# Optimization experiments

Hardware: AMD Instinct MI355X
Metric: run time of the kernel (lower is better)

The kernel has to match this reference:

```python
import jax, jax.numpy as jnp
import numpy as np

PENALTY = -100.0  # reset penalty used by the torch module


def log_g(x):
    # torch: where(x >= 0, log(relu(x) + 0.5), -softplus(-x))
    return jnp.where(x >= 0, jnp.log(jax.nn.relu(x) + 0.5), -jax.nn.softplus(-x))


def setup_inputs() -> dict:
    key = jax.random.key(0)
    k1, k2, k3 = jax.random.split(key, 3)
    B, S, D = 4, 8192, 1024
    x = jax.random.normal(k1, (B, S, D), dtype=jnp.float32)
    W = jax.random.normal(k2, (D, 2 * D), dtype=jnp.float32) * (1.0 / np.sqrt(D))
    input_ids = jax.random.randint(k3, (B, S), 0, 32000, dtype=jnp.int64)
    return {"x": x, "W": W, "input_ids": input_ids}


def reference(x, W, input_ids):
    # x: [B,S,D], W: [D,2D] (to_hidden_and_gate, no bias), proj_out=False -> Identity
    hg = jnp.einsum("bsd,de->bse", x, W)            # [B,S,2D]
    hidden, gate = jnp.split(hg, 2, axis=-1)          # each [B,S,D]

    pad_mask = input_ids == 0                         # [B,S]

    log_coeffs = -jax.nn.softplus(gate)               # log(1 - z)
    log_z = -jax.nn.softplus(-gate)                   # log z
    log_values = log_z + log_g(hidden)                # log(z * h_tilde)

    # reset at positions following a pad token (shifted mask)
    reset = jnp.pad(pad_mask[:, :-1], ((0, 0), (1, 0)))[:, :, None]  # [B,S,1]

    lc = jnp.where(reset, PENALTY, log_coeffs)
    a_star = jnp.cumsum(lc, axis=1)
    lv = jnp.where(reset, PENALTY, log_values)
    log_h = a_star + jax.lax.cumlogsumexp(lv - a_star, axis=1)
    out = jnp.exp(log_h)                              # [B,S,D]

    next_prev_hidden = jnp.where(pad_mask[:, -1:, None], 0.0, out[:, -1:])
    return out, next_prev_hidden
```

## Files before the change

### kernel.cpp

```cpp
#include <hip/hip_runtime.h>
#include <hip/hip_fp16.h>
#include <math.h>

#define S_LEN 8192
#define D_DIM 1024
#define B_DIM 4
#define M_DIM (B_DIM * S_LEN)
#define BSD   ((size_t)M_DIM * D_DIM)
#define CHN   (B_DIM * D_DIM)
#define CHUNK 64
#define NCH   (S_LEN / CHUNK)

typedef _Float16 f16x8 __attribute__((ext_vector_type(8)));
typedef __attribute__((ext_vector_type(4))) float f32x4;
typedef unsigned int u32;

__device__ __forceinline__ u32 pk2h(float a, float b) {
    auto h = __builtin_amdgcn_cvt_pkrtz(a, b);
    u32 r; __builtin_memcpy(&r, &h, 4); return r;
}

__device__ __forceinline__ void gload16(const void* g, void* l) {
    __builtin_amdgcn_global_load_lds(
        (const __attribute__((address_space(1))) u32*)g,
        (__attribute__((address_space(3))) u32*)l,
        16, 0, 0);
}

__global__ __launch_bounds__(256) void w_to_f16t(
    const float* __restrict__ W, unsigned short* __restrict__ Wt)
{
    __shared__ float T[64][65];
    const int t  = threadIdx.x;
    const int n0 = (int)blockIdx.x * 64;
    const int k0 = (int)blockIdx.y * 64;
    #pragma unroll
    for (int p = 0; p < 4; ++p) {
        int u = p * 256 + t;
        int r = u >> 4, c4 = (u & 15) * 4;
        float4 v = *(const float4*)&W[(size_t)(k0 + r) * 2048 + n0 + c4];
        T[r][c4 + 0] = v.x; T[r][c4 + 1] = v.y;
        T[r][c4 + 2] = v.z; T[r][c4 + 3] = v.w;
    }
    __syncthreads();
    #pragma unroll
    for (int p = 0; p < 2; ++p) {
        int u = p * 256 + t;
        int n = u >> 3, kc = (u & 7) * 8;
        u32 out[4];
        #pragma unroll
        for (int j = 0; j < 4; ++j)
            out[j] = pk2h(T[kc + 2 * j][n], T[kc + 2 * j + 1][n]);
        *(uint4*)&Wt[(size_t)(n0 + n) * 1024 + k0 + kc] = *(uint4*)out;
    }
}

__global__ __launch_bounds__(256) void x_to_f16sw(
    const float* __restrict__ x, unsigned short* __restrict__ xh)
{
    int tid = (int)blockIdx.x * 256 + threadIdx.x;
    int m  = tid >> 7;
    int cg = tid & 127;
    const float4* src = (const float4*)&x[(size_t)m * 1024 + cg * 8];
    float4 v0 = src[0], v1 = src[1];
    u32 o[4] = { pk2h(v0.x, v0.y), pk2h(v0.z, v0.w),
                 pk2h(v1.x, v1.y), pk2h(v1.z, v1.w) };
    int j   = cg & 7;
    int cgd = (cg & ~7) | (j ^ (m & 7));
    *(uint4*)&xh[(size_t)m * 1024 + cgd * 8] = *(uint4*)o;
}

__global__ __launch_bounds__(512, 2) void gemm_8p(
    const unsigned short* __restrict__ xh, const unsigned short* __restrict__ Wt,
    const int* __restrict__ ids, u32* __restrict__ P)
{
    __shared__ __align__(16) unsigned short Ah[2 * 256 * 64];

    const int t    = threadIdx.x;
    const int lane = t & 63;
    const int wid  = t >> 6;
    const int wm   = wid >> 2;
    const int wd   = wid & 3;

    const int lin  = (int)blockIdx.x;
    const int xcd  = lin & 7;
    const int slot = lin >> 3;
    const int m0   = (xcd * 16 + (slot >> 3)) * 256;
    const int c0   = (slot & 7) * 128;

    f32x4 accH[8][2], accG[8][2];
    #pragma unroll
    for (int i = 0; i < 8; ++i)
        #pragma unroll
        for (int j = 0; j < 2; ++j) {
            accH[i][j] = (f32x4)0.0f;
            accG[i][j] = (f32x4)0.0f;
        }

    auto stageA = [&](int kb, int buf, int half) {
        char* Ad = (char*)Ah + (buf << 15) + (half << 14);
        #pragma unroll
        for (int i = 0; i < 2; ++i) {
            int sl  = i * 512 + t;
            int row = half * 128 + (sl >> 3);
            int c   = sl & 7;
            const unsigned short* src =
                xh + ((size_t)(m0 + row) << 10) + kb + (c << 3);
            gload16(src, Ad + (size_t)sl * 16);
        }
    };

    auto readA = [&](const char* Ab, int kk, f16x8 a[8]) {
        int chunk = kk * 4 + (lane >> 4);
        #pragma unroll
        for (int mf = 0; mf < 8; ++mf) {
            int row = wm * 128 + mf * 16 + (lane & 15);
            a[mf] = *(const f16x8*)(Ab + row * 128 + ((chunk ^ (row & 7)) << 4));
        }
    };

    auto loadB = [&](f16x8 b[2], int kb, int kk, int hg) {
        int chunk = kk * 4 + (lane >> 4);
        #pragma unroll
        for (int df = 0; df < 2; ++df) {
            int col = wd * 32 + df * 16 + (lane & 15);
            b[df] = *(const f16x8*)(Wt + ((size_t)(hg * 1024 + c0 + col) << 10)
                                       + kb + (chunk << 3));
        }
    };

    #define MMA_CLUSTER(ACC, AV, BV)                                       \
        __builtin_amdgcn_s_setprio(1);                                     \
        _Pragma("unroll")                                                  \
        for (int mf = 0; mf < 8; ++mf)                                     \
            _Pragma("unroll")                                              \
            for (int df = 0; df < 2; ++df)                                 \
                ACC[mf][df] = __builtin_amdgcn_mfma_f32_16x16x32_f16(      \
                    AV[mf], BV[df], ACC[mf][df], 0, 0, 0);                 \
        __builtin_amdgcn_s_setprio(0);

    f16x8 a0[8], a1[8], bh0[2], bg0[2], bh1[2], bg1[2];

    loadB(bh0, 0, 0, 0); loadB(bg0, 0, 0, 1); loadB(bh1, 0, 1, 0);
    stageA(0, 0, 0); stageA(0, 0, 1);
    asm volatile("s_waitcnt vmcnt(0)" ::: "memory");
    __builtin_amdgcn_sched_barrier(0);
    __builtin_amdgcn_s_barrier();

    for (int tt = 0; tt < 16; ++tt) {
        const int buf   = tt & 1;
        const int kbc   = tt << 6;
        const int kbn   = (tt + 1) << 6;
        const bool more = tt < 15;
        const char* Ab = (const char*)Ah + (buf << 15);

        if (tt) { MMA_CLUSTER(accG, a1, bg1) }
        loadB(bg1, kbc, 1, 1);
        if (more) { stageA(kbn, buf ^ 1, 0); stageA(kbn, buf ^ 1, 1); }
        readA(Ab, 0, a0);
        asm volatile("s_waitcnt lgkmcnt(0)" ::: "memory");
        __builtin_amdgcn_sched_barrier(0);
        MMA_CLUSTER(accH, a0, bh0)
        if (more) loadB(bh0, kbn, 0, 0);
        readA(Ab, 1, a1);
        MMA_CLUSTER(accG, a0, bg0)
        if (more) loadB(bg0, kbn, 0, 1);
        asm volatile("s_waitcnt lgkmcnt(0)" ::: "memory");
        __builtin_amdgcn_sched_barrier(0);
        MMA_CLUSTER(accH, a1, bh1)
        if (more) loadB(bh1, kbn, 1, 0);
        if (more) {
            asm volatile("s_waitcnt vmcnt(6)" ::: "memory");
            __builtin_amdgcn_sched_barrier(0);
            __builtin_amdgcn_s_barrier();
        }
    }
    MMA_CLUSTER(accG, a1, bg1)
    #undef MMA_CLUSTER

    #pragma unroll
    for (int mf = 0; mf < 8; ++mf) {
        int mbase = m0 + wm * 128 + mf * 16 + (lane >> 4) * 4;
        #pragma unroll
        for (int r = 0; r < 4; ++r) {
            int m = mbase + r;
            int b = m >> 13;
            int s = m & 8191;
            bool reset = (s > 0) && (ids[b * S_LEN + s - 1] == 0);
            #pragma unroll
            for (int df = 0; df < 2; ++df) {
                int d = c0 + wd * 32 + df * 16 + (lane & 15);
                float hid = accH[mf][df][r];
                float g   = accG[mf][df][r];
                float eg  = __expf(-g);
                float z   = 1.0f / (1.0f + eg);
                float c   = eg * z;
                float gt  = (hid >= 0.0f) ? (hid + 0.5f)
                                          : 1.0f / (1.0f + __expf(-hid));
                float v   = z * gt;
                if (reset) { c = 0.0f; v = 0.0f; }
                __half2 h2 = __floats2half2_rn(c, v);
                u32 packed;
                __builtin_memcpy(&packed, &h2, 4);
                P[(size_t)m * D_DIM + d] = packed;
            }
        }
    }
}

__global__ __launch_bounds__(256, 3) void gemm_fb(
    const float* __restrict__ x, const unsigned short* __restrict__ Wt,
    const int* __restrict__ ids, u32* __restrict__ P)
{
    __shared__ __align__(16) unsigned short Ah[128 * 64];
    __shared__ __align__(16) unsigned short Bt[2 * 64 * 64];

    const int t    = threadIdx.x;
    const int lane = t & 63;
    const int wid  = t >> 6;
    const int wm   = wid >> 1;
    const int wd   = wid & 1;

    const int lin  = (int)blockIdx.y * (int)gridDim.x + (int)blockIdx.x;
    const int xcd  = lin & 7;
    const int slot = lin >> 3;
    const int m0   = (xcd * 32 + (slot >> 4)) * 128;
    const int c0   = (slot & 15) * 64;

    f32x4 accH[4][2], accG[4][2];
    #pragma unroll
    for (int i = 0; i < 4; ++i)
        #pragma unroll
        for (int j = 0; j < 2; ++j) {
            accH[i][j] = (f32x4)0.0f;
            accG[i][j] = (f32x4)0.0f;
        }

    for (int kb = 0; kb < 1024; kb += 64) {
        __syncthreads();
        #pragma unroll
        for (int i = 0; i < 4; ++i) {
            int slotb = wid * 256 + i * 64;
            int sl  = slotb + lane;
            int hg  = sl >> 9;
            int col = (sl >> 3) & 63;
            int kc  = (sl & 7) ^ (col & 7);
            const unsigned short* src =
                Wt + ((size_t)(hg * 1024 + c0 + col) << 10) + kb + (kc << 3);
            gload16(src, (char*)Bt + (size_t)slotb * 16);
        }
        #pragma unroll
        for (int p = 0; p < 8; ++p) {
            int s   = p * 256 + t;
            int row = s >> 4;
            int c4  = s & 15;
            float4 v = *(const float4*)&x[(size_t)(m0 + row) * 1024 + kb + c4 * 4];
            uint2 h;
            h.x = pk2h(v.x, v.y);
            h.y = pk2h(v.z, v.w);
            int byte = row * 128 + ((((c4 >> 1) ^ (row & 7))) << 4) + ((c4 & 1) << 3);
            *(uint2*)((char*)Ah + byte) = h;
        }
        __syncthreads();
        #pragma unroll
        for (int kk = 0; kk < 2; ++kk) {
            f16x8 bh[2], bg[2];
            #pragma unroll
            for (int df = 0; df < 2; ++df) {
                int col = wd * 32 + df * 16 + (lane & 15);
                int chunk = kk * 4 + (lane >> 4);
                int byte = col * 128 + ((chunk ^ (col & 7)) << 4);
                bh[df] = *(const f16x8*)((const char*)Bt + byte);
                bg[df] = *(const f16x8*)((const char*)Bt + 8192 + byte);
            }
            #pragma unroll
            for (int mf = 0; mf < 4; ++mf) {
                int row = wm * 64 + mf * 16 + (lane & 15);
                int chunk = kk * 4 + (lane >> 4);
                int byte = row * 128 + ((chunk ^ (row & 7)) << 4);
                f16x8 a = *(const f16x8*)((const char*)Ah + byte);
                #pragma unroll
                for (int df = 0; df < 2; ++df) {
                    accH[mf][df] = __builtin_amdgcn_mfma_f32_16x16x32_f16(
                        a, bh[df], accH[mf][df], 0, 0, 0);
                    accG[mf][df] = __builtin_amdgcn_mfma_f32_16x16x32_f16(
                        a, bg[df], accG[mf][df], 0, 0, 0);
                }
            }
        }
    }

    #pragma unroll
    for (int mf = 0; mf < 4; ++mf) {
        int mbase = m0 + wm * 64 + mf * 16 + (lane >> 4) * 4;
        #pragma unroll
        for (int r = 0; r < 4; ++r) {
            int m = mbase + r;
            int b = m >> 13;
            int s = m & 8191;
            bool reset = (s > 0) && (ids[b * S_LEN + s - 1] == 0);
            #pragma unroll
            for (int df = 0; df < 2; ++df) {
                int d = c0 + wd * 32 + df * 16 + (lane & 15);
                float hid = accH[mf][df][r];
                float g   = accG[mf][df][r];
                float eg  = __expf(-g);
                float z   = 1.0f / (1.0f + eg);
                float c   = eg * z;
                float gt  = (hid >= 0.0f) ? (hid + 0.5f)
                                          : 1.0f / (1.0f + __expf(-hid));
                float v   = z * gt;
                if (reset) { c = 0.0f; v = 0.0f; }
                __half2 h2 = __floats2half2_rn(c, v);
                u32 packed;
                __builtin_memcpy(&packed, &h2, 4);
                P[(size_t)m * D_DIM + d] = packed;
            }
        }
    }
}

__global__ __launch_bounds__(256) void scan_phase_a(
    const u32* __restrict__ P,
    float* __restrict__ Cp, float* __restrict__ Lp)
{
    int ch0 = (blockIdx.x * 256 + threadIdx.x) * 4;
    int c   = blockIdx.y;
    int b   = ch0 >> 10;
    int d0  = ch0 & 1023;
    size_t base = (size_t)b * S_LEN * D_DIM + d0;
    int s0 = c * CHUNK;

    float C[4] = {1.f, 1.f, 1.f, 1.f};
    float H[4] = {0.f, 0.f, 0.f, 0.f};
    for (int s = 0; s < CHUNK; ++s) {
        uint4 q = *(const uint4*)&P[base + (size_t)(s0 + s) * D_DIM];
        u32 qs[4] = {q.x, q.y, q.z, q.w};
        #pragma unroll
        for (int j = 0; j < 4; ++j) {
            __half2 h2;
            __builtin_memcpy(&h2, &qs[j], 4);
            float cc = __low2float(h2);
            float vv = __high2float(h2);
            H[j] = fmaf(cc, H[j], vv);
            C[j] *= cc;
        }
    }
    *(float4*)&Cp[c * CHN + ch0] = *(float4*)C;
    *(float4*)&Lp[c * CHN + ch0] = *(float4*)H;
}

__global__ __launch_bounds__(256) void scan_phase_b(
    const float* __restrict__ Cp, const float* __restrict__ Lp,
    float* __restrict__ carry)
{
    int ch = blockIdx.x * 256 + threadIdx.x;
    float h = 0.0f;
    for (int c = 0; c < NCH; ++c) {
        carry[c * CHN + ch] = h;
        h = fmaf(Cp[c * CHN + ch], h, Lp[c * CHN + ch]);
    }
}

__global__ __launch_bounds__(256) void scan_phase_c(
    u32* __restrict__ Pio,
    const float* __restrict__ carry,
    const int* __restrict__ ids)
{
    int ch0 = (blockIdx.x * 256 + threadIdx.x) * 4;
    int c   = blockIdx.y;
    int b   = ch0 >> 10;
    int d0  = ch0 & 1023;
    size_t base = (size_t)b * S_LEN * D_DIM + d0;
    int s0 = c * CHUNK;

    float H[4];
    *(float4*)H = *(const float4*)&carry[c * CHN + ch0];

    for (int s = 0; s < CHUNK; ++s) {
        size_t idx = base + (size_t)(s0 + s) * D_DIM;
        uint4 q = *(const uint4*)&Pio[idx];
        u32 qs[4] = {q.x, q.y, q.z, q.w};
        u32 os[4];
        #pragma unroll
        for (int j = 0; j < 4; ++j) {
            __half2 h2;
            __builtin_memcpy(&h2, &qs[j], 4);
            float cc = __low2float(h2);
            float vv = __high2float(h2);
            H[j] = fmaf(cc, H[j], vv);
            os[j] = __float_as_uint(H[j]);
        }
        *(uint4*)&Pio[idx] = *(uint4*)os;
    }
    if (c == NCH - 1) {
        bool pad = (ids[b * S_LEN + (S_LEN - 1)] == 0);
        u32 os[4];
        #pragma unroll
        for (int j = 0; j < 4; ++j)
            os[j] = __float_as_uint(pad ? 0.0f : H[j]);
        *(uint4*)&Pio[BSD + (size_t)b * D_DIM + d0] = *(uint4*)os;
    }
}

extern "C" void kernel_launch(void* const* d_in, const int* in_sizes, int n_in,
                              void* d_out, int out_size, void* d_ws, size_t ws_size,
                              hipStream_t stream) {
    const float* x   = (const float*)d_in[0];
    const float* W   = (const float*)d_in[1];
    const int*   ids = (const int*)d_in[2];

    u32* P = (u32*)d_out;
    unsigned short* Wt = (unsigned short*)d_ws;
    float* Cp    = (float*)((char*)d_ws + (size_t) 4 * 1024 * 1024);
    float* Lp    = (float*)((char*)d_ws + (size_t) 6 * 1024 * 1024);
    float* carry = (float*)((char*)d_ws + (size_t) 8 * 1024 * 1024);
    unsigned short* xh = (unsigned short*)((char*)d_ws + (size_t)10 * 1024 * 1024);
    const size_t need = (size_t)10 * 1024 * 1024 + BSD * 2;

    w_to_f16t<<<dim3(32, 16), 256, 0, stream>>>(W, Wt);

    if (ws_size >= need) {
        x_to_f16sw<<<(M_DIM * 128) / 256, 256, 0, stream>>>(x, xh);
        gemm_8p<<<1024, 512, 0, stream>>>(xh, Wt, ids, P);
    } else {
        dim3 ggrid(D_DIM / 64, M_DIM / 128);
        gemm_fb<<<ggrid, 256, 0, stream>>>(x, Wt, ids, P);
    }

    dim3 sgrid(CHN / 1024, NCH);
    scan_phase_a<<<sgrid, 256, 0, stream>>>(P, Cp, Lp);
    scan_phase_b<<<CHN / 256, 256, 0, stream>>>(Cp, Lp, carry);
    scan_phase_c<<<sgrid, 256, 0, stream>>>(P, carry, ids);
}
```

Before: 304.5 us.

## Restructure fused GEMM to stage both A and B tiles through LDS

Replaces the 512-thread GEMM, which read B fragments directly from global memory with a 64-wide k step, with a 256-thread kernel that stages both x and W tiles into LDS with a 32-wide k step and double buffering. The block tile narrows to 64 output columns, the grid doubles, and the block-to-XCD mapping now assigns columns by XCD. The XOR swizzle on x is removed. The goal is to cut redundant global B loads and simplify the pipeline, but dropping the swizzle risks LDS bank conflicts on the 64-byte row stride, and the full vmcnt(0) wait each iteration reduces overlap between loads and MFMA.

Result: slower. 312.9 us (+2.8%).

```diff
diff --git a/kernel.cpp b/kernel.cpp
--- a/kernel.cpp
+++ b/kernel.cpp
@@ -55,7 +55,7 @@
     }
 }
 
-__global__ __launch_bounds__(256) void x_to_f16sw(
+__global__ __launch_bounds__(256) void x_to_f16(
     const float* __restrict__ x, unsigned short* __restrict__ xh)
 {
     int tid = (int)blockIdx.x * 256 + threadIdx.x;
@@ -65,28 +65,27 @@
     float4 v0 = src[0], v1 = src[1];
     u32 o[4] = { pk2h(v0.x, v0.y), pk2h(v0.z, v0.w),
                  pk2h(v1.x, v1.y), pk2h(v1.z, v1.w) };
-    int j   = cg & 7;
-    int cgd = (cg & ~7) | (j ^ (m & 7));
-    *(uint4*)&xh[(size_t)m * 1024 + cgd * 8] = *(uint4*)o;
-}
-
-__global__ __launch_bounds__(512, 2) void gemm_8p(
+    *(uint4*)&xh[(size_t)m * 1024 + cg * 8] = *(uint4*)o;
+}
+
+__global__ __launch_bounds__(256, 2) void gemm_dc(
     const unsigned short* __restrict__ xh, const unsigned short* __restrict__ Wt,
     const int* __restrict__ ids, u32* __restrict__ P)
 {
-    __shared__ __align__(16) unsigned short Ah[2 * 256 * 64];
+    __shared__ __align__(16) unsigned short Ah[2 * 256 * 32];
+    __shared__ __align__(16) unsigned short Bh[2 * 128 * 32];
 
     const int t    = threadIdx.x;
     const int lane = t & 63;
     const int wid  = t >> 6;
-    const int wm   = wid >> 2;
-    const int wd   = wid & 3;
+    const int wm   = wid >> 1;
+    const int wd   = wid & 1;
 
     const int lin  = (int)blockIdx.x;
     const int xcd  = lin & 7;
     const int slot = lin >> 3;
-    const int m0   = (xcd * 16 + (slot >> 3)) * 256;
-    const int c0   = (slot & 7) * 128;
+    const int m0   = (slot & 127) * 256;
+    const int c0   = (((slot >> 7) << 3) | xcd) * 64;
 
     f32x4 accH[8][2], accG[8][2];
     #pragma unroll
@@ -97,35 +96,44 @@
             accG[i][j] = (f32x4)0.0f;
         }
 
-    auto stageA = [&](int kb, int buf, int half) {
-        char* Ad = (char*)Ah + (buf << 15) + (half << 14);
-        #pragma unroll
-        for (int i = 0; i < 2; ++i) {
-            int sl  = i * 512 + t;
-            int row = half * 128 + (sl >> 3);
-            int c   = sl & 7;
+    auto stageA = [&](int kb, int buf) {
+        char* Ad = (char*)Ah + buf * 16384;
+        #pragma unroll
+        for (int i = 0; i < 4; ++i) {
+            int sl  = i * 256 + t;
+            int row = sl >> 2;
+            int c   = sl & 3;
             const unsigned short* src =
                 xh + ((size_t)(m0 + row) << 10) + kb + (c << 3);
-            gload16(src, Ad + (size_t)sl * 16);
+            gload16(src, Ad + sl * 16);
         }
     };
-
-    auto readA = [&](const char* Ab, int kk, f16x8 a[8]) {
-        int chunk = kk * 4 + (lane >> 4);
+    auto stageB = [&](int kb, int buf) {
+        char* Bd = (char*)Bh + buf * 8192;
+        #pragma unroll
+        for (int i = 0; i < 2; ++i) {
+            int sl  = i * 256 + t;
+            int row = sl >> 2;
+            int c   = sl & 3;
+            int grow = (row >> 6) * 1024 + c0 + (row & 63);
+            const unsigned short* src =
+                Wt + ((size_t)grow << 10) + kb + (c << 3);
+            gload16(src, Bd + sl * 16);
+        }
+    };
+
+    auto readA = [&](const char* Ab, f16x8 a[8]) {
         #pragma unroll
         for (int mf = 0; mf < 8; ++mf) {
             int row = wm * 128 + mf * 16 + (lane & 15);
-            a[mf] = *(const f16x8*)(Ab + row * 128 + ((chunk ^ (row & 7)) << 4));
+            a[mf] = *(const f16x8*)(Ab + row * 64 + ((lane >> 4) << 4));
         }
     };
-
-    auto loadB = [&](f16x8 b[2], int kb, int kk, int hg) {
-        int chunk = kk * 4 + (lane >> 4);
+    auto readB = [&](const char* Bb, int hg, f16x8 b[2]) {
         #pragma unroll
         for (int df = 0; df < 2; ++df) {
-            int col = wd * 32 + df * 16 + (lane & 15);
-            b[df] = *(const f16x8*)(Wt + ((size_t)(hg * 1024 + c0 + col) << 10)
-                                       + kb + (chunk << 3));
+            int row = hg * 64 + wd * 32 + df * 16 + (lane & 15);
+            b[df] = *(const f16x8*)(Bb + row * 64 + ((lane >> 4) << 4));
         }
     };
 
@@ -139,43 +147,32 @@
                     AV[mf], BV[df], ACC[mf][df], 0, 0, 0);                 \
         __builtin_amdgcn_s_setprio(0);
 
-    f16x8 a0[8], a1[8], bh0[2], bg0[2], bh1[2], bg1[2];
-
-    loadB(bh0, 0, 0, 0); loadB(bg0, 0, 0, 1); loadB(bh1, 0, 1, 0);
-    stageA(0, 0, 0); stageA(0, 0, 1);
+    stageA(0, 0); stageB(0, 0);
     asm volatile("s_waitcnt vmcnt(0)" ::: "memory");
     __builtin_amdgcn_sched_barrier(0);
     __builtin_amdgcn_s_barrier();
 
-    for (int tt = 0; tt < 16; ++tt) {
+    for (int tt = 0; tt < 32; ++tt) {
         const int buf   = tt & 1;
-        const int kbc   = tt << 6;
-        const int kbn   = (tt + 1) << 6;
-        const bool more = tt < 15;
-        const char* Ab = (const char*)Ah + (buf << 15);
-
-        if (tt) { MMA_CLUSTER(accG, a1, bg1) }
-        loadB(bg1, kbc, 1, 1);
-        if (more) { stageA(kbn, buf ^ 1, 0); stageA(kbn, buf ^ 1, 1); }
-        readA(Ab, 0, a0);
+        const bool more = tt < 31;
+        const char* Ab = (const char*)Ah + buf * 16384;
+        const char* Bb = (const char*)Bh + buf * 8192;
+        f16x8 a[8], bh[2], bg[2];
+
+        if (more) { stageA((tt + 1) * 32, buf ^ 1); stageB((tt + 1) * 32, buf ^ 1); }
+        readA(Ab, a); readB(Bb, 0, bh); readB(Bb, 1, bg);
+        asm volatile("s_waitcnt lgkmcnt(2)" ::: "memory");
+        __builtin_amdgcn_sched_barrier(0);
+        MMA_CLUSTER(accH, a, bh)
         asm volatile("s_waitcnt lgkmcnt(0)" ::: "memory");
         __builtin_amdgcn_sched_barrier(0);
-        MMA_CLUSTER(accH, a0, bh0)
-        if (more) loadB(bh0, kbn, 0, 0);
-        readA(Ab, 1, a1);
-        MMA_CLUSTER(accG, a0, bg0)
-        if (more) loadB(bg0, kbn, 0, 1);
-        asm volatile("s_waitcnt lgkmcnt(0)" ::: "memory");
-        __builtin_amdgcn_sched_barrier(0);
-        MMA_CLUSTER(accH, a1, bh1)
-        if (more) loadB(bh1, kbn, 1, 0);
+        MMA_CLUSTER(accG, a, bg)
         if (more) {
-            asm volatile("s_waitcnt vmcnt(6)" ::: "memory");
+            asm volatile("s_waitcnt vmcnt(0)" ::: "memory");
             __builtin_amdgcn_sched_barrier(0);
             __builtin_amdgcn_s_barrier();
         }
     }
-    MMA_CLUSTER(accG, a1, bg1)
     #undef MMA_CLUSTER
 
     #pragma unroll
@@ -421,8 +418,8 @@
     w_to_f16t<<<dim3(32, 16), 256, 0, stream>>>(W, Wt);
 
     if (ws_size >= need) {
-        x_to_f16sw<<<(M_DIM * 128) / 256, 256, 0, stream>>>(x, xh);
-        gemm_8p<<<1024, 512, 0, stream>>>(xh, Wt, ids, P);
+        x_to_f16<<<(M_DIM * 128) / 256, 256, 0, stream>>>(x, xh);
+        gemm_dc<<<2048, 256, 0, stream>>>(xh, Wt, ids, P);
     } else {
         dim3 ggrid(D_DIM / 64, M_DIM / 128);
         gemm_fb<<<ggrid, 256, 0, stream>>>(x, Wt, ids, P);
```

## Fuse chunk-scan phase A into fallback GEMM epilogue and drop f16-x GEMM path

Applied to the files above, without the earlier changes.

Removes the x-to-f16 conversion kernel and the tuned 8-wave GEMM, so the direct-from-f32 fallback GEMM always runs. Its epilogue now computes per-64-row chunk affine summaries (cumulative coefficient product and local state) through a shared-memory reduction and writes Cp/Lp directly. This removes scan_phase_a and its full reread of P. The trade-off is that the fallback GEMM is likely less efficient than the pipelined 8-wave kernel it replaces.

Result: faster. 287.6 us (-5.5%).

```diff
diff --git a/kernel.cpp b/kernel.cpp
--- a/kernel.cpp
+++ b/kernel.cpp
@@ -55,165 +55,14 @@
     }
 }
 
-__global__ __launch_bounds__(256) void x_to_f16sw(
-    const float* __restrict__ x, unsigned short* __restrict__ xh)
-{
-    int tid = (int)blockIdx.x * 256 + threadIdx.x;
-    int m  = tid >> 7;
-    int cg = tid & 127;
-    const float4* src = (const float4*)&x[(size_t)m * 1024 + cg * 8];
-    float4 v0 = src[0], v1 = src[1];
-    u32 o[4] = { pk2h(v0.x, v0.y), pk2h(v0.z, v0.w),
-                 pk2h(v1.x, v1.y), pk2h(v1.z, v1.w) };
-    int j   = cg & 7;
-    int cgd = (cg & ~7) | (j ^ (m & 7));
-    *(uint4*)&xh[(size_t)m * 1024 + cgd * 8] = *(uint4*)o;
-}
-
-__global__ __launch_bounds__(512, 2) void gemm_8p(
-    const unsigned short* __restrict__ xh, const unsigned short* __restrict__ Wt,
-    const int* __restrict__ ids, u32* __restrict__ P)
-{
-    __shared__ __align__(16) unsigned short Ah[2 * 256 * 64];
-
-    const int t    = threadIdx.x;
-    const int lane = t & 63;
-    const int wid  = t >> 6;
-    const int wm   = wid >> 2;
-    const int wd   = wid & 3;
-
-    const int lin  = (int)blockIdx.x;
-    const int xcd  = lin & 7;
-    const int slot = lin >> 3;
-    const int m0   = (xcd * 16 + (slot >> 3)) * 256;
-    const int c0   = (slot & 7) * 128;
-
-    f32x4 accH[8][2], accG[8][2];
-    #pragma unroll
-    for (int i = 0; i < 8; ++i)
-        #pragma unroll
-        for (int j = 0; j < 2; ++j) {
-            accH[i][j] = (f32x4)0.0f;
-            accG[i][j] = (f32x4)0.0f;
-        }
-
-    auto stageA = [&](int kb, int buf, int half) {
-        char* Ad = (char*)Ah + (buf << 15) + (half << 14);
-        #pragma unroll
-        for (int i = 0; i < 2; ++i) {
-            int sl  = i * 512 + t;
-            int row = half * 128 + (sl >> 3);
-            int c   = sl & 7;
-            const unsigned short* src =
-                xh + ((size_t)(m0 + row) << 10) + kb + (c << 3);
-            gload16(src, Ad + (size_t)sl * 16);
-        }
-    };
-
-    auto readA = [&](const char* Ab, int kk, f16x8 a[8]) {
-        int chunk = kk * 4 + (lane >> 4);
-        #pragma unroll
-        for (int mf = 0; mf < 8; ++mf) {
-            int row = wm * 128 + mf * 16 + (lane & 15);
-            a[mf] = *(const f16x8*)(Ab + row * 128 + ((chunk ^ (row & 7)) << 4));
-        }
-    };
-
-    auto loadB = [&](f16x8 b[2], int kb, int kk, int hg) {
-        int chunk = kk * 4 + (lane >> 4);
-        #pragma unroll
-        for (int df = 0; df < 2; ++df) {
-            int col = wd * 32 + df * 16 + (lane & 15);
-            b[df] = *(const f16x8*)(Wt + ((size_t)(hg * 1024 + c0 + col) << 10)
-                                       + kb + (chunk << 3));
-        }
-    };
-
-    #define MMA_CLUSTER(ACC, AV, BV)                                       \
-        __builtin_amdgcn_s_setprio(1);                                     \
-        _Pragma("unroll")                                                  \
-        for (int mf = 0; mf < 8; ++mf)                                     \
-            _Pragma("unroll")                                              \
-            for (int df = 0; df < 2; ++df)                                 \
-                ACC[mf][df] = __builtin_amdgcn_mfma_f32_16x16x32_f16(      \
-                    AV[mf], BV[df], ACC[mf][df], 0, 0, 0);                 \
-        __builtin_amdgcn_s_setprio(0);
-
-    f16x8 a0[8], a1[8], bh0[2], bg0[2], bh1[2], bg1[2];
-
-    loadB(bh0, 0, 0, 0); loadB(bg0, 0, 0, 1); loadB(bh1, 0, 1, 0);
-    stageA(0, 0, 0); stageA(0, 0, 1);
-    asm volatile("s_waitcnt vmcnt(0)" ::: "memory");
-    __builtin_amdgcn_sched_barrier(0);
-    __builtin_amdgcn_s_barrier();
-
-    for (int tt = 0; tt < 16; ++tt) {
-        const int buf   = tt & 1;
-        const int kbc   = tt << 6;
-        const int kbn   = (tt + 1) << 6;
-        const bool more = tt < 15;
-        const char* Ab = (const char*)Ah + (buf << 15);
-
-        if (tt) { MMA_CLUSTER(accG, a1, bg1) }
-        loadB(bg1, kbc, 1, 1);
-        if (more) { stageA(kbn, buf ^ 1, 0); stageA(kbn, buf ^ 1, 1); }
-        readA(Ab, 0, a0);
-        asm volatile("s_waitcnt lgkmcnt(0)" ::: "memory");
-        __builtin_amdgcn_sched_barrier(0);
-        MMA_CLUSTER(accH, a0, bh0)
-        if (more) loadB(bh0, kbn, 0, 0);
-        readA(Ab, 1, a1);
-        MMA_CLUSTER(accG, a0, bg0)
-        if (more) loadB(bg0, kbn, 0, 1);
-        asm volatile("s_waitcnt lgkmcnt(0)" ::: "memory");
-        __builtin_amdgcn_sched_barrier(0);
-        MMA_CLUSTER(accH, a1, bh1)
-        if (more) loadB(bh1, kbn, 1, 0);
-        if (more) {
-            asm volatile("s_waitcnt vmcnt(6)" ::: "memory");
-            __builtin_amdgcn_sched_barrier(0);
-            __builtin_amdgcn_s_barrier();
-        }
-    }
-    MMA_CLUSTER(accG, a1, bg1)
-    #undef MMA_CLUSTER
-
-    #pragma unroll
-    for (int mf = 0; mf < 8; ++mf) {
-        int mbase = m0 + wm * 128 + mf * 16 + (lane >> 4) * 4;
-        #pragma unroll
-        for (int r = 0; r < 4; ++r) {
-            int m = mbase + r;
-            int b = m >> 13;
-            int s = m & 8191;
-            bool reset = (s > 0) && (ids[b * S_LEN + s - 1] == 0);
-            #pragma unroll
-            for (int df = 0; df < 2; ++df) {
-                int d = c0 + wd * 32 + df * 16 + (lane & 15);
-                float hid = accH[mf][df][r];
-                float g   = accG[mf][df][r];
-                float eg  = __expf(-g);
-                float z   = 1.0f / (1.0f + eg);
-                float c   = eg * z;
-                float gt  = (hid >= 0.0f) ? (hid + 0.5f)
-                                          : 1.0f / (1.0f + __expf(-hid));
-                float v   = z * gt;
-                if (reset) { c = 0.0f; v = 0.0f; }
-                __half2 h2 = __floats2half2_rn(c, v);
-                u32 packed;
-                __builtin_memcpy(&packed, &h2, 4);
-                P[(size_t)m * D_DIM + d] = packed;
-            }
-        }
-    }
-}
-
 __global__ __launch_bounds__(256, 3) void gemm_fb(
     const float* __restrict__ x, const unsigned short* __restrict__ Wt,
-    const int* __restrict__ ids, u32* __restrict__ P)
+    const int* __restrict__ ids, u32* __restrict__ P,
+    float* __restrict__ Cp, float* __restrict__ Lp)
 {
     __shared__ __align__(16) unsigned short Ah[128 * 64];
     __shared__ __align__(16) unsigned short Bt[2 * 64 * 64];
+    __shared__ float Caff[2][16][64][2];
 
     const int t    = threadIdx.x;
     const int lane = t & 63;
@@ -293,6 +142,8 @@
     #pragma unroll
     for (int mf = 0; mf < 4; ++mf) {
         int mbase = m0 + wm * 64 + mf * 16 + (lane >> 4) * 4;
+        float Cr[2] = {1.0f, 1.0f};
+        float Lr[2] = {0.0f, 0.0f};
         #pragma unroll
         for (int r = 0; r < 4; ++r) {
             int m = mbase + r;
@@ -315,39 +166,37 @@
                 u32 packed;
                 __builtin_memcpy(&packed, &h2, 4);
                 P[(size_t)m * D_DIM + d] = packed;
+                Lr[df] = fmaf(c, Lr[df], v);
+                Cr[df] *= c;
             }
         }
-    }
-}
-
-__global__ __launch_bounds__(256) void scan_phase_a(
-    const u32* __restrict__ P,
-    float* __restrict__ Cp, float* __restrict__ Lp)
-{
-    int ch0 = (blockIdx.x * 256 + threadIdx.x) * 4;
-    int c   = blockIdx.y;
-    int b   = ch0 >> 10;
-    int d0  = ch0 & 1023;
-    size_t base = (size_t)b * S_LEN * D_DIM + d0;
-    int s0 = c * CHUNK;
-
-    float C[4] = {1.f, 1.f, 1.f, 1.f};
-    float H[4] = {0.f, 0.f, 0.f, 0.f};
-    for (int s = 0; s < CHUNK; ++s) {
-        uint4 q = *(const uint4*)&P[base + (size_t)(s0 + s) * D_DIM];
-        u32 qs[4] = {q.x, q.y, q.z, q.w};
-        #pragma unroll
-        for (int j = 0; j < 4; ++j) {
-            __half2 h2;
-            __builtin_memcpy(&h2, &qs[j], 4);
-            float cc = __low2float(h2);
-            float vv = __high2float(h2);
-            H[j] = fmaf(cc, H[j], vv);
-            C[j] *= cc;
-        }
-    }
-    *(float4*)&Cp[c * CHN + ch0] = *(float4*)C;
-    *(float4*)&Lp[c * CHN + ch0] = *(float4*)H;
+        int rq = mf * 4 + (lane >> 4);
+        #pragma unroll
+        for (int df = 0; df < 2; ++df) {
+            int col = wd * 32 + df * 16 + (lane & 15);
+            Caff[wm][rq][col][0] = Cr[df];
+            Caff[wm][rq][col][1] = Lr[df];
+        }
+    }
+    __syncthreads();
+    if (t < 128) {
+        int sc  = t >> 6;
+        int col = t & 63;
+        float C = 1.0f, L = 0.0f;
+        #pragma unroll
+        for (int q = 0; q < 16; ++q) {
+            float cq = Caff[sc][q][col][0];
+            float lq = Caff[sc][q][col][1];
+            L = fmaf(cq, L, lq);
+            C *= cq;
+        }
+        int m    = m0 + sc * 64;
+        int b    = m >> 13;
+        int cidx = (m & 8191) >> 6;
+        int ch   = (b << 10) | (c0 + col);
+        Cp[cidx * CHN + ch] = C;
+        Lp[cidx * CHN + ch] = L;
+    }
 }
 
 __global__ __launch_bounds__(256) void scan_phase_b(
@@ -415,21 +264,13 @@
     float* Cp    = (float*)((char*)d_ws + (size_t) 4 * 1024 * 1024);
     float* Lp    = (float*)((char*)d_ws + (size_t) 6 * 1024 * 1024);
     float* carry = (float*)((char*)d_ws + (size_t) 8 * 1024 * 1024);
-    unsigned short* xh = (unsigned short*)((char*)d_ws + (size_t)10 * 1024 * 1024);
-    const size_t need = (size_t)10 * 1024 * 1024 + BSD * 2;
 
     w_to_f16t<<<dim3(32, 16), 256, 0, stream>>>(W, Wt);
 
-    if (ws_size >= need) {
-        x_to_f16sw<<<(M_DIM * 128) / 256, 256, 0, stream>>>(x, xh);
-        gemm_8p<<<1024, 512, 0, stream>>>(xh, Wt, ids, P);
-    } else {
-        dim3 ggrid(D_DIM / 64, M_DIM / 128);
-        gemm_fb<<<ggrid, 256, 0, stream>>>(x, Wt, ids, P);
-    }
+    dim3 ggrid(D_DIM / 64, M_DIM / 128);
+    gemm_fb<<<ggrid, 256, 0, stream>>>(x, Wt, ids, P, Cp, Lp);
 
     dim3 sgrid(CHN / 1024, NCH);
-    scan_phase_a<<<sgrid, 256, 0, stream>>>(P, Cp, Lp);
     scan_phase_b<<<CHN / 256, 256, 0, stream>>>(Cp, Lp, carry);
     scan_phase_c<<<sgrid, 256, 0, stream>>>(P, carry, ids);
 }
```
